# Optimization experiments

Hardware: AMD Instinct MI355X
Metric: run time of the kernel (lower is better)

## Reference

```python
import jax, jax.numpy as jnp
import numpy as np

T, N = 1000, 4096            # seq len, batch
N_STATE, N_DIST = 16, 8      # state / disturbance feature dims
H, L = 8, 2                  # lstm hidden, lstm layers
DEC, N_ACTION = 4, 4         # decoder hidden, action dim


def _unif(k, shape, fan):
    b = 1.0 / np.sqrt(fan)
    return jax.random.uniform(k, shape, jnp.float32, -b, b)


def setup_inputs() -> dict:
    key = jax.random.key(0)
    ks = jax.random.split(key, 24)
    inp = {
        "state": jax.random.normal(ks[0], (N, N_STATE), jnp.float32),
        "disturbance": jax.random.normal(ks[1], (T, N, N_DIST), jnp.float32),
        # encoder1: n_state -> 4 -> H*L (=16)
        "enc1_W1": _unif(ks[2], (4, N_STATE), N_STATE), "enc1_b1": _unif(ks[3], (4,), N_STATE),
        "enc1_W2": _unif(ks[4], (H * L, 4), 4),          "enc1_b2": _unif(ks[5], (H * L,), 4),
        # encoder2
        "enc2_W1": _unif(ks[6], (4, N_STATE), N_STATE), "enc2_b1": _unif(ks[7], (4,), N_STATE),
        "enc2_W2": _unif(ks[8], (H * L, 4), 4),          "enc2_b2": _unif(ks[9], (H * L,), 4),
        # LSTM layer 0 (input N_DIST) and layer 1 (input H); gate order i,f,g,o
        "W_ih0": _unif(ks[10], (4 * H, N_DIST), H), "W_hh0": _unif(ks[11], (4 * H, H), H),
        "b_ih0": _unif(ks[12], (4 * H,), H),        "b_hh0": _unif(ks[13], (4 * H,), H),
        "W_ih1": _unif(ks[14], (4 * H, H), H),      "W_hh1": _unif(ks[15], (4 * H, H), H),
        "b_ih1": _unif(ks[16], (4 * H,), H),        "b_hh1": _unif(ks[17], (4 * H,), H),
        # decoder: H -> DEC, then two heads DEC -> N_ACTION
        "dec_W": _unif(ks[18], (DEC, H), H),        "dec_b": _unif(ks[19], (DEC,), H),
        "fin_W": _unif(ks[20], (N_ACTION, DEC), DEC),  "fin_b": _unif(ks[21], (N_ACTION,), DEC),
        "fin2_W": _unif(ks[22], (N_ACTION, DEC), DEC), "fin2_b": _unif(ks[23], (N_ACTION,), DEC),
    }
    return inp


def _lstm_layer(x, h0, c0, W_ih, W_hh, b_ih, b_hh):
    # x: [T, n, d_in] -> out: [T, n, H]. Precompute input-side gates once.
    xg = jnp.einsum('tnd,gd->tng', x, W_ih) + b_ih + b_hh  # [T, n, 4H]

    def step(carry, xg_t):
        h, c = carry
        g = xg_t + h @ W_hh.T
        i, f, gg, o = jnp.split(g, 4, axis=-1)
        c = jax.nn.sigmoid(f) * c + jax.nn.sigmoid(i) * jnp.tanh(gg)
        h = jax.nn.sigmoid(o) * jnp.tanh(c)
        return (h, c), h

    _, out = jax.lax.scan(step, (h0, c0), xg)
    return out


def reference(state, disturbance,
              enc1_W1, enc1_b1, enc1_W2, enc1_b2,
              enc2_W1, enc2_b1, enc2_W2, enc2_b2,
              W_ih0, W_hh0, b_ih0, b_hh0,
              W_ih1, W_hh1, b_ih1, b_hh1,
              dec_W, dec_b, fin_W, fin_b, fin2_W, fin2_b):
    n = state.shape[0]

    def enc(W1, b1, W2, b2):
        h = jax.nn.relu(state @ W1.T + b1)
        h = jax.nn.relu(h @ W2.T + b2)
        return h.reshape(n, L, H).transpose(1, 0, 2)  # [L, n, H]

    h0 = enc(enc1_W1, enc1_b1, enc1_W2, enc1_b2)
    c0 = enc(enc2_W1, enc2_b1, enc2_W2, enc2_b2)

    out = _lstm_layer(disturbance, h0[0], c0[0], W_ih0, W_hh0, b_ih0, b_hh0)
    out = _lstm_layer(out,         h0[1], c0[1], W_ih1, W_hh1, b_ih1, b_hh1)

    dec = jax.nn.relu(out @ dec_W.T + dec_b)          # [T, n, DEC]
    mu = dec @ fin_W.T + fin_b                        # [T, n, N_ACTION]
    sigma_sq = dec @ fin2_W.T + fin2_b
    return mu, sigma_sq
```

## Files before the change

### kernel.cpp

```cpp
#include <hip/hip_runtime.h>

namespace {

constexpr int T_STEPS = 1000;
constexpr int NB      = 4096;
constexpr float LOG2E = 1.4426950408889634f;

typedef float v2f __attribute__((ext_vector_type(2)));

__device__ __forceinline__ float fexp2(float x) { return __builtin_amdgcn_exp2f(x); }
__device__ __forceinline__ float frcp(float x)  { return __builtin_amdgcn_rcpf(x); }

__device__ __forceinline__ v2f mkv2(float a, float b) { v2f r; r.x = a; r.y = b; return r; }

__device__ __forceinline__ v2f pkfma(v2f a, v2f b, v2f c) {
#if __has_builtin(__builtin_elementwise_fma)
    return __builtin_elementwise_fma(a, b, c);
#else
    v2f r; r.x = fmaf(a.x, b.x, c.x); r.y = fmaf(a.y, b.y, c.y); return r;
#endif
}

template<int CTRL>
__device__ __forceinline__ float dppf(float v) {
    int i = __float_as_int(v);
    return __int_as_float(__builtin_amdgcn_update_dpp(i, i, CTRL, 0xF, 0xF, false));
}

__global__ __launch_bounds__(256, 1)
void lstm_fused_kernel(
    const float* __restrict__ state, const float* __restrict__ dist,
    const float* __restrict__ e1W1, const float* __restrict__ e1b1,
    const float* __restrict__ e1W2, const float* __restrict__ e1b2,
    const float* __restrict__ e2W1, const float* __restrict__ e2b1,
    const float* __restrict__ e2W2, const float* __restrict__ e2b2,
    const float* __restrict__ Wih0, const float* __restrict__ Whh0,
    const float* __restrict__ bih0, const float* __restrict__ bhh0,
    const float* __restrict__ Wih1, const float* __restrict__ Whh1,
    const float* __restrict__ bih1, const float* __restrict__ bhh1,
    const float* __restrict__ decW, const float* __restrict__ decb,
    const float* __restrict__ finW, const float* __restrict__ finb,
    const float* __restrict__ fin2W, const float* __restrict__ fin2b,
    float* __restrict__ out)
{
    const int tid = (int)threadIdx.x;
    const int q   = tid & 15;
    const int n   = blockIdx.x * 16 + (tid >> 4);
    const int u   = q & 7;
    const int hlf = q >> 3;
    const int r0  = hlf * 16 + u;
    const int r1  = r0 + 8;

    const int pv  = __builtin_amdgcn_update_dpp(0, q, 0x121, 0xF, 0xF, true);
    const int sgn = (pv == ((q + 1) & 15)) ? 1 : -1;
    auto pidx = [&](int k) { return (u + sgn * k) & 7; };

    const float sA   = hlf ? (-2.0f * LOG2E) : (-LOG2E);
    const float sB   = -LOG2E;
    const float mulA = hlf ? 2.0f : 1.0f;
    const float addA = hlf ? -1.0f : 0.0f;

    v2f wx0a[4], wh0a[4], wx0b[4], wh0b[4];
    v2f wx1a[4], wh1a[4], wx1b[4], wh1b[4];
#pragma unroll
    for (int k = 0; k < 4; ++k) {
        const int k0 = 2 * k, k1 = 2 * k + 1;
        const int p0 = pidx(k0), p1 = pidx(k1);
        wx0a[k] = mkv2(Wih0[r0 * 8 + k0] * sA, Wih0[r0 * 8 + k1] * sA);
        wh0a[k] = mkv2(Whh0[r0 * 8 + p0] * sA, Whh0[r0 * 8 + p1] * sA);
        wx0b[k] = mkv2(Wih0[r1 * 8 + k0] * sB, Wih0[r1 * 8 + k1] * sB);
        wh0b[k] = mkv2(Whh0[r1 * 8 + p0] * sB, Whh0[r1 * 8 + p1] * sB);
        wx1a[k] = mkv2(Wih1[r0 * 8 + p0] * sA, Wih1[r0 * 8 + p1] * sA);
        wh1a[k] = mkv2(Whh1[r0 * 8 + p0] * sA, Whh1[r0 * 8 + p1] * sA);
        wx1b[k] = mkv2(Wih1[r1 * 8 + p0] * sB, Wih1[r1 * 8 + p1] * sB);
        wh1b[k] = mkv2(Whh1[r1 * 8 + p0] * sB, Whh1[r1 * 8 + p1] * sB);
    }
    const float bA0 = (bih0[r0] + bhh0[r0]) * sA, bB0 = (bih0[r1] + bhh0[r1]) * sB;
    const float bA1 = (bih1[r0] + bhh1[r0]) * sA, bB1 = (bih1[r1] + bhh1[r1]) * sB;

    const int dr = q & 3;
    v2f dwr2[4];
#pragma unroll
    for (int k = 0; k < 4; ++k)
        dwr2[k] = mkv2(decW[dr * 8 + pidx(2 * k)], decW[dr * 8 + pidx(2 * k + 1)]);
    const float db = decb[dr];
    float fwp[4]; float fb;
    {
        const float* Wp = (u < 4) ? finW : fin2W;
        const float* bp = (u < 4) ? finb : fin2b;
        const int oo = u & 3;
#pragma unroll
        for (int jj = 0; jj < 4; ++jj) fwp[jj] = Wp[oo * 4 + ((dr + jj) & 3)];
        fb = bp[oo];
    }

    float h0s[8], h1s[8], c0, c1;
    {
        float s[16];
#pragma unroll
        for (int k = 0; k < 16; ++k) s[k] = state[n * 16 + k];
        float hm1[4], hm2[4];
#pragma unroll
        for (int m = 0; m < 4; ++m) {
            float a = e1b1[m], b = e2b1[m];
#pragma unroll
            for (int k = 0; k < 16; ++k) {
                a = fmaf(s[k], e1W1[m * 16 + k], a);
                b = fmaf(s[k], e2W1[m * 16 + k], b);
            }
            hm1[m] = fmaxf(a, 0.0f); hm2[m] = fmaxf(b, 0.0f);
        }
#pragma unroll
        for (int k = 0; k < 8; ++k) {
            const int p = pidx(k);
            float a = e1b2[p], b = e1b2[8 + p];
#pragma unroll
            for (int m = 0; m < 4; ++m) {
                a = fmaf(hm1[m], e1W2[p * 4 + m], a);
                b = fmaf(hm1[m], e1W2[(8 + p) * 4 + m], b);
            }
            h0s[k] = fmaxf(a, 0.0f);
            h1s[k] = fmaxf(b, 0.0f);
        }
        float a = e2b2[u], b = e2b2[8 + u];
#pragma unroll
        for (int m = 0; m < 4; ++m) {
            a = fmaf(hm2[m], e2W2[u * 4 + m], a);
            b = fmaf(hm2[m], e2W2[(8 + u) * 4 + m], b);
        }
        c0 = fmaxf(a, 0.0f);
        c1 = fmaxf(b, 0.0f);
    }
    v2f h0r0 = mkv2(h0s[0], h0s[1]), h0r1 = mkv2(h0s[2], h0s[3]);
    v2f h0r2 = mkv2(h0s[4], h0s[5]), h0r3 = mkv2(h0s[6], h0s[7]);
    v2f h1r0 = mkv2(h1s[0], h1s[1]), h1r1 = mkv2(h1s[2], h1s[3]);
    v2f h1r2 = mkv2(h1s[4], h1s[5]), h1r3 = mkv2(h1s[6], h1s[7]);

    const float4* dp = reinterpret_cast<const float4*>(dist) + (size_t)n * 2;
    constexpr size_t TS4 = (size_t)NB * 2;
    float* outp = out + ((u < 4) ? ((size_t)n * 4 + u)
                                 : ((size_t)T_STEPS * NB * 4 + (size_t)n * 4 + (u - 4)));
    const bool doStore = (q < 8);

    auto step = [&](const float4& lo, const float4& hi, float* op) {
        const v2f x0 = mkv2(lo.x, lo.y), x1 = mkv2(lo.z, lo.w);
        const v2f x2 = mkv2(hi.x, hi.y), x3 = mkv2(hi.z, hi.w);
        v2f pa = pkfma(x0, wx0a[0], mkv2(bA0, 0.0f));
        pa = pkfma(x1, wx0a[1], pa);
        pa = pkfma(h0r0, wh0a[0], pa);
        pa = pkfma(h0r1, wh0a[1], pa);
        v2f qa = pkfma(x2, wx0a[2], mkv2(0.0f, 0.0f));
        qa = pkfma(x3, wx0a[3], qa);
        qa = pkfma(h0r2, wh0a[2], qa);
        qa = pkfma(h0r3, wh0a[3], qa);
        v2f sa = pa + qa;
        const float A = sa.x + sa.y;
        v2f pb = pkfma(x0, wx0b[0], mkv2(bB0, 0.0f));
        pb = pkfma(x1, wx0b[1], pb);
        pb = pkfma(h0r0, wh0b[0], pb);
        pb = pkfma(h0r1, wh0b[1], pb);
        v2f qb = pkfma(x2, wx0b[2], mkv2(0.0f, 0.0f));
        qb = pkfma(x3, wx0b[3], qb);
        qb = pkfma(h0r2, wh0b[2], qb);
        qb = pkfma(h0r3, wh0b[3], qb);
        v2f sb = pb + qb;
        const float B = sb.x + sb.y;
        float a0 = fmaf(frcp(1.0f + fexp2(A)), mulA, addA);
        float a1 = frcp(1.0f + fexp2(B));
        float s0 = dppf<0x128>(a0);
        float s1 = dppf<0x128>(a1);
        float prod = a0 * s0;
        float fg = hlf ? s1 : a1, og = hlf ? a1 : s1;
        c0 = fmaf(fg, c0, prod);
        float th = fmaf(frcp(1.0f + fexp2(c0 * (-2.0f * LOG2E))), 2.0f, -1.0f);
        float hn = og * th;
        {
            const float t1 = dppf<0x121>(hn), t2 = dppf<0x122>(hn), t3 = dppf<0x123>(hn);
            const float t4 = dppf<0x124>(hn), t5 = dppf<0x125>(hn), t6 = dppf<0x126>(hn);
            const float t7 = dppf<0x127>(hn);
            h0r0 = mkv2(hn, t1); h0r1 = mkv2(t2, t3);
            h0r2 = mkv2(t4, t5); h0r3 = mkv2(t6, t7);
        }
        v2f pa1 = pkfma(h1r0, wh1a[0], mkv2(bA1, 0.0f));
        pa1 = pkfma(h1r1, wh1a[1], pa1);
        pa1 = pkfma(h0r0, wx1a[0], pa1);
        pa1 = pkfma(h0r1, wx1a[1], pa1);
        v2f qa1 = pkfma(h1r2, wh1a[2], mkv2(0.0f, 0.0f));
        qa1 = pkfma(h1r3, wh1a[3], qa1);
        qa1 = pkfma(h0r2, wx1a[2], qa1);
        qa1 = pkfma(h0r3, wx1a[3], qa1);
        v2f sa1 = pa1 + qa1;
        const float A1 = sa1.x + sa1.y;
        v2f pb1 = pkfma(h1r0, wh1b[0], mkv2(bB1, 0.0f));
        pb1 = pkfma(h1r1, wh1b[1], pb1);
        pb1 = pkfma(h0r0, wx1b[0], pb1);
        pb1 = pkfma(h0r1, wx1b[1], pb1);
        v2f qb1 = pkfma(h1r2, wh1b[2], mkv2(0.0f, 0.0f));
        qb1 = pkfma(h1r3, wh1b[3], qb1);
        qb1 = pkfma(h0r2, wx1b[2], qb1);
        qb1 = pkfma(h0r3, wx1b[3], qb1);
        v2f sb1 = pb1 + qb1;
        const float B1 = sb1.x + sb1.y;
        a0 = fmaf(frcp(1.0f + fexp2(A1)), mulA, addA);
        a1 = frcp(1.0f + fexp2(B1));
        s0 = dppf<0x128>(a0);
        s1 = dppf<0x128>(a1);
        prod = a0 * s0;
        fg = hlf ? s1 : a1; og = hlf ? a1 : s1;
        c1 = fmaf(fg, c1, prod);
        th = fmaf(frcp(1.0f + fexp2(c1 * (-2.0f * LOG2E))), 2.0f, -1.0f);
        hn = og * th;
        {
            const float t1 = dppf<0x121>(hn), t2 = dppf<0x122>(hn), t3 = dppf<0x123>(hn);
            const float t4 = dppf<0x124>(hn), t5 = dppf<0x125>(hn), t6 = dppf<0x126>(hn);
            const float t7 = dppf<0x127>(hn);
            h1r0 = mkv2(hn, t1); h1r1 = mkv2(t2, t3);
            h1r2 = mkv2(t4, t5); h1r3 = mkv2(t6, t7);
        }
        v2f dd = pkfma(h1r0, dwr2[0], mkv2(db, 0.0f));
        dd = pkfma(h1r1, dwr2[1], dd);
        v2f de = pkfma(h1r2, dwr2[2], mkv2(0.0f, 0.0f));
        de = pkfma(h1r3, dwr2[3], de);
        v2f dsum = dd + de;
        float da = fmaxf(dsum.x + dsum.y, 0.0f);
        const float d1 = dppf<0x39>(da);
        const float d2 = dppf<0x4E>(da);
        const float d3 = dppf<0x93>(da);
        float o = fb;
        o = fmaf(da, fwp[0], o); o = fmaf(d1, fwp[1], o);
        o = fmaf(d2, fwp[2], o); o = fmaf(d3, fwp[3], o);
        if (doStore) *op = o;
    };

    float4 r0a = dp[0],       r0b = dp[1];
    float4 r1a = dp[TS4],     r1b = dp[TS4 + 1];
    float4 r2a = dp[2 * TS4], r2b = dp[2 * TS4 + 1];
    float4 r3a = dp[3 * TS4], r3b = dp[3 * TS4 + 1];
    const float4* pf = dp + 4 * TS4;

    for (int it = 0; it < 249; ++it) {
        float4 na, nb;
        na = pf[0]; nb = pf[1]; pf += TS4;
        step(r0a, r0b, outp); outp += (size_t)NB * 4;
        r0a = na; r0b = nb;
        na = pf[0]; nb = pf[1]; pf += TS4;
        step(r1a, r1b, outp); outp += (size_t)NB * 4;
        r1a = na; r1b = nb;
        na = pf[0]; nb = pf[1]; pf += TS4;
        step(r2a, r2b, outp); outp += (size_t)NB * 4;
        r2a = na; r2b = nb;
        na = pf[0]; nb = pf[1]; pf += TS4;
        step(r3a, r3b, outp); outp += (size_t)NB * 4;
        r3a = na; r3b = nb;
    }
    step(r0a, r0b, outp); outp += (size_t)NB * 4;
    step(r1a, r1b, outp); outp += (size_t)NB * 4;
    step(r2a, r2b, outp); outp += (size_t)NB * 4;
    step(r3a, r3b, outp);
}

}

extern "C" void kernel_launch(void* const* d_in, const int* in_sizes, int n_in,
                              void* d_out, int out_size, void* d_ws, size_t ws_size,
                              hipStream_t stream) {
    const float* state = (const float*)d_in[0];
    const float* dist  = (const float*)d_in[1];
    const float* e1W1  = (const float*)d_in[2];
    const float* e1b1  = (const float*)d_in[3];
    const float* e1W2  = (const float*)d_in[4];
    const float* e1b2  = (const float*)d_in[5];
    const float* e2W1  = (const float*)d_in[6];
    const float* e2b1  = (const float*)d_in[7];
    const float* e2W2  = (const float*)d_in[8];
    const float* e2b2  = (const float*)d_in[9];
    const float* Wih0  = (const float*)d_in[10];
    const float* Whh0  = (const float*)d_in[11];
    const float* bih0  = (const float*)d_in[12];
    const float* bhh0  = (const float*)d_in[13];
    const float* Wih1  = (const float*)d_in[14];
    const float* Whh1  = (const float*)d_in[15];
    const float* bih1  = (const float*)d_in[16];
    const float* bhh1  = (const float*)d_in[17];
    const float* decW  = (const float*)d_in[18];
    const float* decb  = (const float*)d_in[19];
    const float* finW  = (const float*)d_in[20];
    const float* finb  = (const float*)d_in[21];
    const float* fin2W = (const float*)d_in[22];
    const float* fin2b = (const float*)d_in[23];
    float* outp = (float*)d_out;

    lstm_fused_kernel<<<dim3(NB / 16), dim3(256), 0, stream>>>(
        state, dist,
        e1W1, e1b1, e1W2, e1b2,
        e2W1, e2b1, e2W2, e2b2,
        Wih0, Whh0, bih0, bhh0,
        Wih1, Whh1, bih1, bhh1,
        decW, decb, finW, finb, fin2W, fin2b,
        outp);
}
```

Before: 317.6 us.

## Skew LSTM layers so layer-0 step t+1 overlaps layer-1 step t

Restructures the per-timestep loop so layer 0 runs one step ahead of layer 1. Layer 0 for step t+1 and layer 1 plus the decoder for step t are then independent and can be interleaved, which shortens the serial dependency chain per iteration. The prefetch depth grows to five timesteps, and the last in-loop prefetch is redirected to a valid address to avoid reading out of bounds. Tanh is also folded into the output-gate multiply with one FMA. The extra live registers may raise register pressure.

```diff
diff --git a/kernel.cpp b/kernel.cpp
--- a/kernel.cpp
+++ b/kernel.cpp
@@ -10,7 +10,6 @@
 
 __device__ __forceinline__ float fexp2(float x) { return __builtin_amdgcn_exp2f(x); }
 __device__ __forceinline__ float frcp(float x)  { return __builtin_amdgcn_rcpf(x); }
-
 __device__ __forceinline__ v2f mkv2(float a, float b) { v2f r; r.x = a; r.y = b; return r; }
 
 __device__ __forceinline__ v2f pkfma(v2f a, v2f b, v2f c) {
@@ -94,7 +93,18 @@
         fb = bp[oo];
     }
 
-    float h0s[8], h1s[8], c0, c1;
+    const float4* dp = reinterpret_cast<const float4*>(dist) + (size_t)n * 2;
+    constexpr size_t TS4 = (size_t)NB * 2;
+    float4 x0a = dp[0],       x0b = dp[1];
+    float4 g0a = dp[TS4],     g0b = dp[TS4 + 1];
+    float4 g1a = dp[2 * TS4], g1b = dp[2 * TS4 + 1];
+    float4 g2a = dp[3 * TS4], g2b = dp[3 * TS4 + 1];
+    float4 g3a = dp[4 * TS4], g3b = dp[4 * TS4 + 1];
+    const float4* pf = dp + 5 * TS4;
+
+    v2f hp0, hp1, hp2, hp3;
+    v2f h10, h11, h12, h13;
+    float c0, c1;
     {
         float s[16];
 #pragma unroll
@@ -110,6 +120,7 @@
             }
             hm1[m] = fmaxf(a, 0.0f); hm2[m] = fmaxf(b, 0.0f);
         }
+        float h0s[8], h1s[8];
 #pragma unroll
         for (int k = 0; k < 8; ++k) {
             const int p = pidx(k);
@@ -130,99 +141,102 @@
         }
         c0 = fmaxf(a, 0.0f);
         c1 = fmaxf(b, 0.0f);
+        hp0 = mkv2(h0s[0], h0s[1]); hp1 = mkv2(h0s[2], h0s[3]);
+        hp2 = mkv2(h0s[4], h0s[5]); hp3 = mkv2(h0s[6], h0s[7]);
+        h10 = mkv2(h1s[0], h1s[1]); h11 = mkv2(h1s[2], h1s[3]);
+        h12 = mkv2(h1s[4], h1s[5]); h13 = mkv2(h1s[6], h1s[7]);
     }
-    v2f h0r0 = mkv2(h0s[0], h0s[1]), h0r1 = mkv2(h0s[2], h0s[3]);
-    v2f h0r2 = mkv2(h0s[4], h0s[5]), h0r3 = mkv2(h0s[6], h0s[7]);
-    v2f h1r0 = mkv2(h1s[0], h1s[1]), h1r1 = mkv2(h1s[2], h1s[3]);
-    v2f h1r2 = mkv2(h1s[4], h1s[5]), h1r3 = mkv2(h1s[6], h1s[7]);
-
-    const float4* dp = reinterpret_cast<const float4*>(dist) + (size_t)n * 2;
-    constexpr size_t TS4 = (size_t)NB * 2;
+
     float* outp = out + ((u < 4) ? ((size_t)n * 4 + u)
                                  : ((size_t)T_STEPS * NB * 4 + (size_t)n * 4 + (u - 4)));
     const bool doStore = (q < 8);
-
-    auto step = [&](const float4& lo, const float4& hi, float* op) {
-        const v2f x0 = mkv2(lo.x, lo.y), x1 = mkv2(lo.z, lo.w);
-        const v2f x2 = mkv2(hi.x, hi.y), x3 = mkv2(hi.z, hi.w);
-        v2f pa = pkfma(x0, wx0a[0], mkv2(bA0, 0.0f));
-        pa = pkfma(x1, wx0a[1], pa);
-        pa = pkfma(h0r0, wh0a[0], pa);
-        pa = pkfma(h0r1, wh0a[1], pa);
-        v2f qa = pkfma(x2, wx0a[2], mkv2(0.0f, 0.0f));
-        qa = pkfma(x3, wx0a[3], qa);
-        qa = pkfma(h0r2, wh0a[2], qa);
-        qa = pkfma(h0r3, wh0a[3], qa);
+    const v2f zero2 = mkv2(0.0f, 0.0f);
+
+    v2f hc0, hc1, hc2, hc3;
+    auto L0body = [&](const float4& lo, const float4& hi) {
+        const v2f X0 = mkv2(lo.x, lo.y), X1 = mkv2(lo.z, lo.w);
+        const v2f X2 = mkv2(hi.x, hi.y), X3 = mkv2(hi.z, hi.w);
+        v2f pa = pkfma(X0, wx0a[0], mkv2(bA0, 0.0f));
+        pa = pkfma(X1, wx0a[1], pa);
+        pa = pkfma(hp0, wh0a[0], pa);
+        pa = pkfma(hp1, wh0a[1], pa);
+        v2f qa = pkfma(X2, wx0a[2], zero2);
+        qa = pkfma(X3, wx0a[3], qa);
+        qa = pkfma(hp2, wh0a[2], qa);
+        qa = pkfma(hp3, wh0a[3], qa);
         v2f sa = pa + qa;
         const float A = sa.x + sa.y;
-        v2f pb = pkfma(x0, wx0b[0], mkv2(bB0, 0.0f));
-        pb = pkfma(x1, wx0b[1], pb);
-        pb = pkfma(h0r0, wh0b[0], pb);
-        pb = pkfma(h0r1, wh0b[1], pb);
-        v2f qb = pkfma(x2, wx0b[2], mkv2(0.0f, 0.0f));
-        qb = pkfma(x3, wx0b[3], qb);
-        qb = pkfma(h0r2, wh0b[2], qb);
-        qb = pkfma(h0r3, wh0b[3], qb);
+        v2f pb = pkfma(X0, wx0b[0], mkv2(bB0, 0.0f));
+        pb = pkfma(X1, wx0b[1], pb);
+        pb = pkfma(hp0, wh0b[0], pb);
+        pb = pkfma(hp1, wh0b[1], pb);
+        v2f qb = pkfma(X2, wx0b[2], zero2);
+        qb = pkfma(X3, wx0b[3], qb);
+        qb = pkfma(hp2, wh0b[2], qb);
+        qb = pkfma(hp3, wh0b[3], qb);
         v2f sb = pb + qb;
         const float B = sb.x + sb.y;
         float a0 = fmaf(frcp(1.0f + fexp2(A)), mulA, addA);
         float a1 = frcp(1.0f + fexp2(B));
-        float s0 = dppf<0x128>(a0);
-        float s1 = dppf<0x128>(a1);
-        float prod = a0 * s0;
-        float fg = hlf ? s1 : a1, og = hlf ? a1 : s1;
+        const float s0 = dppf<0x128>(a0);
+        const float s1 = dppf<0x128>(a1);
+        const float prod = a0 * s0;
+        const float fg = hlf ? s1 : a1;
+        const float og = hlf ? a1 : s1;
         c0 = fmaf(fg, c0, prod);
-        float th = fmaf(frcp(1.0f + fexp2(c0 * (-2.0f * LOG2E))), 2.0f, -1.0f);
-        float hn = og * th;
-        {
-            const float t1 = dppf<0x121>(hn), t2 = dppf<0x122>(hn), t3 = dppf<0x123>(hn);
-            const float t4 = dppf<0x124>(hn), t5 = dppf<0x125>(hn), t6 = dppf<0x126>(hn);
-            const float t7 = dppf<0x127>(hn);
-            h0r0 = mkv2(hn, t1); h0r1 = mkv2(t2, t3);
-            h0r2 = mkv2(t4, t5); h0r3 = mkv2(t6, t7);
-        }
-        v2f pa1 = pkfma(h1r0, wh1a[0], mkv2(bA1, 0.0f));
-        pa1 = pkfma(h1r1, wh1a[1], pa1);
-        pa1 = pkfma(h0r0, wx1a[0], pa1);
-        pa1 = pkfma(h0r1, wx1a[1], pa1);
-        v2f qa1 = pkfma(h1r2, wh1a[2], mkv2(0.0f, 0.0f));
-        qa1 = pkfma(h1r3, wh1a[3], qa1);
-        qa1 = pkfma(h0r2, wx1a[2], qa1);
-        qa1 = pkfma(h0r3, wx1a[3], qa1);
-        v2f sa1 = pa1 + qa1;
-        const float A1 = sa1.x + sa1.y;
-        v2f pb1 = pkfma(h1r0, wh1b[0], mkv2(bB1, 0.0f));
-        pb1 = pkfma(h1r1, wh1b[1], pb1);
-        pb1 = pkfma(h0r0, wx1b[0], pb1);
-        pb1 = pkfma(h0r1, wx1b[1], pb1);
-        v2f qb1 = pkfma(h1r2, wh1b[2], mkv2(0.0f, 0.0f));
-        qb1 = pkfma(h1r3, wh1b[3], qb1);
-        qb1 = pkfma(h0r2, wx1b[2], qb1);
-        qb1 = pkfma(h0r3, wx1b[3], qb1);
-        v2f sb1 = pb1 + qb1;
-        const float B1 = sb1.x + sb1.y;
-        a0 = fmaf(frcp(1.0f + fexp2(A1)), mulA, addA);
-        a1 = frcp(1.0f + fexp2(B1));
-        s0 = dppf<0x128>(a0);
-        s1 = dppf<0x128>(a1);
-        prod = a0 * s0;
-        fg = hlf ? s1 : a1; og = hlf ? a1 : s1;
+        const float rr  = frcp(1.0f + fexp2(c0 * (-2.0f * LOG2E)));
+        const float og2 = og + og;
+        const float hn  = fmaf(og2, rr, -og);
+        const float t1 = dppf<0x121>(hn), t2 = dppf<0x122>(hn), t3 = dppf<0x123>(hn);
+        const float t4 = dppf<0x124>(hn), t5 = dppf<0x125>(hn), t6 = dppf<0x126>(hn);
+        const float t7 = dppf<0x127>(hn);
+        hc0 = mkv2(hn, t1); hc1 = mkv2(t2, t3);
+        hc2 = mkv2(t4, t5); hc3 = mkv2(t6, t7);
+    };
+
+    auto L1decBody = [&](float* op) {
+        v2f pa = pkfma(hp0, wx1a[0], mkv2(bA1, 0.0f));
+        pa = pkfma(hp1, wx1a[1], pa);
+        pa = pkfma(h10, wh1a[0], pa);
+        pa = pkfma(h11, wh1a[1], pa);
+        v2f qa = pkfma(hp2, wx1a[2], zero2);
+        qa = pkfma(hp3, wx1a[3], qa);
+        qa = pkfma(h12, wh1a[2], qa);
+        qa = pkfma(h13, wh1a[3], qa);
+        v2f sa = pa + qa;
+        const float A = sa.x + sa.y;
+        v2f pb = pkfma(hp0, wx1b[0], mkv2(bB1, 0.0f));
+        pb = pkfma(hp1, wx1b[1], pb);
+        pb = pkfma(h10, wh1b[0], pb);
+        pb = pkfma(h11, wh1b[1], pb);
+        v2f qb = pkfma(hp2, wx1b[2], zero2);
+        qb = pkfma(hp3, wx1b[3], qb);
+        qb = pkfma(h12, wh1b[2], qb);
+        qb = pkfma(h13, wh1b[3], qb);
+        v2f sb = pb + qb;
+        const float B = sb.x + sb.y;
+        float a0 = fmaf(frcp(1.0f + fexp2(A)), mulA, addA);
+        float a1 = frcp(1.0f + fexp2(B));
+        const float s0 = dppf<0x128>(a0);
+        const float s1 = dppf<0x128>(a1);
+        const float prod = a0 * s0;
+        const float fg = hlf ? s1 : a1;
+        const float og = hlf ? a1 : s1;
         c1 = fmaf(fg, c1, prod);
-        th = fmaf(frcp(1.0f + fexp2(c1 * (-2.0f * LOG2E))), 2.0f, -1.0f);
-        hn = og * th;
-        {
-            const float t1 = dppf<0x121>(hn), t2 = dppf<0x122>(hn), t3 = dppf<0x123>(hn);
-            const float t4 = dppf<0x124>(hn), t5 = dppf<0x125>(hn), t6 = dppf<0x126>(hn);
-            const float t7 = dppf<0x127>(hn);
-            h1r0 = mkv2(hn, t1); h1r1 = mkv2(t2, t3);
-            h1r2 = mkv2(t4, t5); h1r3 = mkv2(t6, t7);
-        }
-        v2f dd = pkfma(h1r0, dwr2[0], mkv2(db, 0.0f));
-        dd = pkfma(h1r1, dwr2[1], dd);
-        v2f de = pkfma(h1r2, dwr2[2], mkv2(0.0f, 0.0f));
-        de = pkfma(h1r3, dwr2[3], de);
-        v2f dsum = dd + de;
-        float da = fmaxf(dsum.x + dsum.y, 0.0f);
+        const float rr  = frcp(1.0f + fexp2(c1 * (-2.0f * LOG2E)));
+        const float og2 = og + og;
+        const float hn  = fmaf(og2, rr, -og);
+        const float t1 = dppf<0x121>(hn), t2 = dppf<0x122>(hn), t3 = dppf<0x123>(hn);
+        const float t4 = dppf<0x124>(hn), t5 = dppf<0x125>(hn), t6 = dppf<0x126>(hn);
+        const float t7 = dppf<0x127>(hn);
+        h10 = mkv2(hn, t1); h11 = mkv2(t2, t3);
+        h12 = mkv2(t4, t5); h13 = mkv2(t6, t7);
+        v2f dd = pkfma(h10, dwr2[0], mkv2(db, 0.0f));
+        dd = pkfma(h11, dwr2[1], dd);
+        v2f de = pkfma(h12, dwr2[2], zero2);
+        de = pkfma(h13, dwr2[3], de);
+        v2f ds = dd + de;
+        float da = fmaxf(ds.x + ds.y, 0.0f);
         const float d1 = dppf<0x39>(da);
         const float d2 = dppf<0x4E>(da);
         const float d3 = dppf<0x93>(da);
@@ -232,31 +246,36 @@
         if (doStore) *op = o;
     };
 
-    float4 r0a = dp[0],       r0b = dp[1];
-    float4 r1a = dp[TS4],     r1b = dp[TS4 + 1];
-    float4 r2a = dp[2 * TS4], r2b = dp[2 * TS4 + 1];
-    float4 r3a = dp[3 * TS4], r3b = dp[3 * TS4 + 1];
-    const float4* pf = dp + 4 * TS4;
+    L0body(x0a, x0b);
+    hp0 = hc0; hp1 = hc1; hp2 = hc2; hp3 = hc3;
 
     for (int it = 0; it < 249; ++it) {
         float4 na, nb;
         na = pf[0]; nb = pf[1]; pf += TS4;
-        step(r0a, r0b, outp); outp += (size_t)NB * 4;
-        r0a = na; r0b = nb;
+        L0body(g0a, g0b); L1decBody(outp); outp += (size_t)NB * 4;
+        hp0 = hc0; hp1 = hc1; hp2 = hc2; hp3 = hc3;
+        g0a = na; g0b = nb;
         na = pf[0]; nb = pf[1]; pf += TS4;
-        step(r1a, r1b, outp); outp += (size_t)NB * 4;
-        r1a = na; r1b = nb;
+        L0body(g1a, g1b); L1decBody(outp); outp += (size_t)NB * 4;
+        hp0 = hc0; hp1 = hc1; hp2 = hc2; hp3 = hc3;
+        g1a = na; g1b = nb;
         na = pf[0]; nb = pf[1]; pf += TS4;
-        step(r2a, r2b, outp); outp += (size_t)NB * 4;
-        r2a = na; r2b = nb;
-        na = pf[0]; nb = pf[1]; pf += TS4;
-        step(r3a, r3b, outp); outp += (size_t)NB * 4;
-        r3a = na; r3b = nb;
+        L0body(g2a, g2b); L1decBody(outp); outp += (size_t)NB * 4;
+        hp0 = hc0; hp1 = hc1; hp2 = hc2; hp3 = hc3;
+        g2a = na; g2b = nb;
+        const float4* pfx = (it == 248) ? dp : pf;
+        na = pfx[0]; nb = pfx[1]; pf += TS4;
+        L0body(g3a, g3b); L1decBody(outp); outp += (size_t)NB * 4;
+        hp0 = hc0; hp1 = hc1; hp2 = hc2; hp3 = hc3;
+        g3a = na; g3b = nb;
     }
-    step(r0a, r0b, outp); outp += (size_t)NB * 4;
-    step(r1a, r1b, outp); outp += (size_t)NB * 4;
-    step(r2a, r2b, outp); outp += (size_t)NB * 4;
-    step(r3a, r3b, outp);
+    L0body(g0a, g0b); L1decBody(outp); outp += (size_t)NB * 4;
+    hp0 = hc0; hp1 = hc1; hp2 = hc2; hp3 = hc3;
+    L0body(g1a, g1b); L1decBody(outp); outp += (size_t)NB * 4;
+    hp0 = hc0; hp1 = hc1; hp2 = hc2; hp3 = hc3;
+    L0body(g2a, g2b); L1decBody(outp); outp += (size_t)NB * 4;
+    hp0 = hc0; hp1 = hc1; hp2 = hc2; hp3 = hc3;
+    L1decBody(outp);
 }
 
 }
```

Result: faster. 307.8 us (-3.1%).
